# Kernel optimization log

Measured on AMD Instinct MI355X. Metric: run time of the kernel, lower is better.

Reference implementation:

```python
import jax, jax.numpy as jnp
import numpy as np

# heavy-atom counts minus 1 (the residue_len) for the 20 standard amino acids
# GLY ALA SER CYS THR VAL PRO LEU ILE ASN ASP MET GLN GLU LYS HIS PHE ARG TYR TRP
NATOMS = np.array([4,5,6,6,7,7,7,8,8,8,8,8,9,9,9,10,11,11,12,14], dtype=np.int64)
NTYPES = 20
MAXA = int(NATOMS.max())  # 14
B, R, VDIM, NLIN = 128, 512, 256, 3


def setup_inputs() -> dict:
    rng = np.random.default_rng(0)
    type_ids = rng.integers(0, NTYPES, size=R)                     # metadata.seq as type ids
    natoms = NATOMS[type_ids]                                      # per-residue atom count
    residue_indices = np.concatenate([[0], np.cumsum(natoms)[:-1]])  # start atom of each residue
    n_atoms = int(natoms.sum())

    key = jax.random.key(0)
    k1, k2, k3 = jax.random.split(key, 3)
    x = jax.random.normal(k1, (B, n_atoms, 3), dtype=jnp.float32)

    # per-type first-layer weight, zero-padded beyond each type's natom so the
    # padded gathered atoms contribute exactly zero (identical math to slicing)
    pad_mask = (np.arange(MAXA)[None, :] < NATOMS[:, None]).astype(np.float32)  # (T, A)
    W0 = jax.random.normal(k2, (NTYPES, VDIM, MAXA), dtype=jnp.float32)
    W0 = W0 * (1.0 / np.sqrt(MAXA)) * jnp.asarray(pad_mask)[:, None, :]
    Wh = jax.random.normal(k3, (NTYPES, NLIN - 1, VDIM, VDIM), dtype=jnp.float32) * (1.0 / np.sqrt(VDIM))

    return {
        "x": x,
        "W0": W0,
        "Wh": Wh,
        "type_ids": jnp.asarray(type_ids, dtype=jnp.int64),
        "residue_indices": jnp.asarray(residue_indices, dtype=jnp.int64),
    }


def reference(x, W0, Wh, type_ids, residue_indices):
    """x:(B, atoms, 3) -> pos_ca:(B, R, 3), x_v:(B, R, VDIM, 3)"""
    n_atoms = x.shape[1]
    # gather each residue's atom window, padded to MAXA (clip keeps indices in
    # range; padded entries are killed by the zero-padded W0 columns)
    atom_idx = jnp.clip(residue_indices[:, None] + jnp.arange(MAXA)[None, :], 0, n_atoms - 1)  # (R, A)
    gathered = x[:, atom_idx]                               # (B, R, A, 3)
    root = x[:, residue_indices + 1]                        # (B, R, 3)  -- CA atom (x[:,1] of each slice)
    delta = gathered - root[:, :, None, :]                  # subtract root

    h = jnp.einsum('rva,brac->brvc', W0[type_ids], delta)   # per-type VecLinear(natom -> vdim)
    for l in range(NLIN - 1):                               # per-type VecLinear(vdim -> vdim)
        h = jnp.einsum('rvu,bruc->brvc', Wh[type_ids, l], h)

    pos_ca = root                                            # x[:, residue_indices + 1]
    return pos_ca, h
```

## Files before the change

kernel.cpp:

```cpp
#include <hip/hip_runtime.h>

namespace {
constexpr int NB = 128;
constexpr int NR = 512;
constexpr int ND = 256;
constexpr int NA = 14;

using short8 = __attribute__((ext_vector_type(8))) short;
using f32x4  = __attribute__((ext_vector_type(4))) float;

constexpr size_t WH_US  = (size_t)40 * 16 * 8 * 64 * 8;
constexpr size_t W0_OFF = WH_US;
constexpr size_t W0_US  = (size_t)20 * 16 * 64 * 8;
constexpr size_t RMAP_BYTE_OFF = (WH_US + W0_US) * 2;
constexpr size_t WS_NEEDED = RMAP_BYTE_OFF + NR * sizeof(int);

__device__ __forceinline__ unsigned short f2bf(float f) {
    unsigned int u = __float_as_uint(f);
    u = (u + 0x7FFFu + ((u >> 16) & 1u)) >> 16;
    return (unsigned short)u;
}
}

__global__ void conv_wh(const float* __restrict__ Wh, unsigned short* __restrict__ ws) {
    int g = blockIdx.x * 256 + threadIdx.x;
    if (g >= 40 * 16 * 8 * 64) return;
    const int lane = g & 63, kt = (g >> 6) & 7, mt = (g >> 9) & 15, tl = g >> 13;
    const int v = mt * 16 + (lane & 15);
    const int u0 = kt * 32 + (lane >> 4) * 8;
    const float* src = Wh + ((size_t)tl * ND + v) * ND + u0;
    unsigned short o[8];
#pragma unroll
    for (int j = 0; j < 8; ++j) o[j] = f2bf(src[j]);
    uint4 pk;
    pk.x = o[0] | ((unsigned)o[1] << 16); pk.y = o[2] | ((unsigned)o[3] << 16);
    pk.z = o[4] | ((unsigned)o[5] << 16); pk.w = o[6] | ((unsigned)o[7] << 16);
    *reinterpret_cast<uint4*>(ws + (size_t)g * 8) = pk;
}

__global__ void conv_w0(const float* __restrict__ W0, unsigned short* __restrict__ ws) {
    int g = blockIdx.x * 256 + threadIdx.x;
    if (g >= 20 * 16 * 64) return;
    const int lane = g & 63, mt = (g >> 6) & 15, t = g >> 10;
    const int v = mt * 16 + (lane & 15);
    const int a0 = (lane >> 4) * 8;
    unsigned short o[8];
#pragma unroll
    for (int j = 0; j < 8; ++j) {
        const int a = a0 + j;
        o[j] = (a < NA) ? f2bf(W0[((size_t)t * ND + v) * NA + a]) : (unsigned short)0;
    }
    uint4 pk;
    pk.x = o[0] | ((unsigned)o[1] << 16); pk.y = o[2] | ((unsigned)o[3] << 16);
    pk.z = o[4] | ((unsigned)o[5] << 16); pk.w = o[6] | ((unsigned)o[7] << 16);
    *reinterpret_cast<uint4*>(ws + W0_OFF + (size_t)g * 8) = pk;
}

__global__ void build_rmap(const int* __restrict__ type_ids, int* __restrict__ rmap) {
    __shared__ int tl[NR];
    const int tid = threadIdx.x;
    tl[tid] = type_ids[tid];
    __syncthreads();
    const int myt = tl[tid];
    int pos = 0;
    for (int j = 0; j < NR; ++j) {
        const int tj = tl[j];
        pos += (tj < myt) || (tj == myt && j < tid);
    }
    rmap[pos] = tid;
}

__global__ __launch_bounds__(512, 6) void residues_mfma(
    const float* __restrict__ x, const unsigned short* __restrict__ wsw,
    const int* __restrict__ rmap, const int* __restrict__ type_ids,
    const int* __restrict__ res_idx, float* __restrict__ out, int n_atoms)
{
    const int tid = threadIdx.x, lane = tid & 63, w = tid >> 6;
    const int xcd = blockIdx.x & 7, j = blockIdx.x >> 3;
    const int r = rmap[xcd * 64 + (j >> 3)];
    const int b0 = (j & 7) * 16;
    const int ri = res_idx[r], t = type_ids[r];

    __shared__ __align__(16) unsigned short HT[48 * 264];
    unsigned short* dltT = HT;

    const unsigned short* w0b = wsw + W0_OFF + (size_t)t * (16 * 64 * 8);
    short8 a0[2];
#pragma unroll
    for (int mi = 0; mi < 2; ++mi)
        a0[mi] = *reinterpret_cast<const short8*>(w0b + (((w * 2 + mi) * 64) + lane) * 8);

    {
        const int bl = tid >> 5, k = tid & 31;
        const float* xb = x + (size_t)(b0 + bl) * n_atoms * 3;
        if (k < 16) {
            int atom = ri + k; if (atom > n_atoms - 1) atom = n_atoms - 1;
            const float* src  = xb + (size_t)atom * 3;
            const float* root = xb + (size_t)(ri + 1) * 3;
#pragma unroll
            for (int c = 0; c < 3; ++c)
                dltT[(bl * 3 + c) * 40 + k] = f2bf(src[c] - root[c]);
            if (k == 1) {
#pragma unroll
                for (int c = 0; c < 3; ++c)
                    out[((size_t)(b0 + bl) * NR + r) * 3 + c] = root[c];
            }
        } else {
#pragma unroll
            for (int c = 0; c < 3; ++c)
                dltT[(bl * 3 + c) * 40 + k] = 0;
        }
    }
    __syncthreads();

    f32x4 acc[2][3];
#pragma unroll
    for (int mi = 0; mi < 2; ++mi)
#pragma unroll
        for (int ni = 0; ni < 3; ++ni) acc[mi][ni] = f32x4{0.f, 0.f, 0.f, 0.f};

    {
        short8 bf[3];
#pragma unroll
        for (int ni = 0; ni < 3; ++ni)
            bf[ni] = *reinterpret_cast<const short8*>(&dltT[(ni * 16 + (lane & 15)) * 40 + (lane >> 4) * 8]);
#pragma unroll
        for (int mi = 0; mi < 2; ++mi)
#pragma unroll
            for (int ni = 0; ni < 3; ++ni)
                acc[mi][ni] = __builtin_amdgcn_mfma_f32_16x16x32_bf16(a0[mi], bf[ni], acc[mi][ni], 0, 0, 0);
    }
    __syncthreads();

#pragma unroll 1
    for (int l = 0; l < 2; ++l) {
#pragma unroll
        for (int mi = 0; mi < 2; ++mi)
#pragma unroll
            for (int ni = 0; ni < 3; ++ni) {
                const int v0 = w * 32 + mi * 16 + (lane >> 4) * 4;
                const int n  = ni * 16 + (lane & 15);
                const unsigned lo = (unsigned)f2bf(acc[mi][ni][0]) | ((unsigned)f2bf(acc[mi][ni][1]) << 16);
                const unsigned hi = (unsigned)f2bf(acc[mi][ni][2]) | ((unsigned)f2bf(acc[mi][ni][3]) << 16);
                *reinterpret_cast<uint2*>(&HT[n * 264 + v0]) = make_uint2(lo, hi);
            }
        __syncthreads();

#pragma unroll
        for (int mi = 0; mi < 2; ++mi)
#pragma unroll
            for (int ni = 0; ni < 3; ++ni) acc[mi][ni] = f32x4{0.f, 0.f, 0.f, 0.f};

        const unsigned short* wl = wsw + (size_t)(t * 2 + l) * (16 * 8 * 64 * 8);
#pragma unroll 1
        for (int kt = 0; kt < 8; ++kt) {
            short8 a[2], bf[3];
#pragma unroll
            for (int mi = 0; mi < 2; ++mi)
                a[mi] = *reinterpret_cast<const short8*>(wl + ((((w * 2 + mi) * 8 + kt) * 64) + lane) * 8);
#pragma unroll
            for (int ni = 0; ni < 3; ++ni)
                bf[ni] = *reinterpret_cast<const short8*>(&HT[(ni * 16 + (lane & 15)) * 264 + kt * 32 + (lane >> 4) * 8]);
#pragma unroll
            for (int mi = 0; mi < 2; ++mi)
#pragma unroll
                for (int ni = 0; ni < 3; ++ni)
                    acc[mi][ni] = __builtin_amdgcn_mfma_f32_16x16x32_bf16(a[mi], bf[ni], acc[mi][ni], 0, 0, 0);
        }
        if (l == 0) __syncthreads();
    }

    float* fst  = reinterpret_cast<float*>(HT);
    float* outh = out + (size_t)NB * NR * 3;
#pragma unroll 1
    for (int p = 0; p < 2; ++p) {
        __syncthreads();
        if ((w >> 2) == p) {
            const int wq = w & 3;
#pragma unroll
            for (int mi = 0; mi < 2; ++mi)
#pragma unroll
                for (int ni = 0; ni < 3; ++ni) {
                    const int n = ni * 16 + (lane & 15);
#pragma unroll
                    for (int jj = 0; jj < 4; ++jj) {
                        const int vl = wq * 32 + mi * 16 + (lane >> 4) * 4 + jj;
                        fst[n * 132 + vl] = acc[mi][ni][jj];
                    }
                }
        }
        __syncthreads();
#pragma unroll
        for (int i = 0; i < 3; ++i) {
            const int idx = tid + i * 512;
            const int bl = idx / 96, g = idx % 96;
            f32x4 v4;
#pragma unroll
            for (int e = 0; e < 4; ++e) {
                const int f = 4 * g + e, c = f % 3, vp = f / 3;
                v4[e] = fst[(bl * 3 + c) * 132 + vp];
            }
            __builtin_nontemporal_store(v4,
                reinterpret_cast<f32x4*>(&outh[(((size_t)(b0 + bl) * NR + r) * (ND * 3)) + p * 384 + 4 * g]));
        }
    }
}

__global__ __launch_bounds__(256, 3) void residues_fused_fb(
    const float* __restrict__ x, const float* __restrict__ W0,
    const float* __restrict__ Wh, const int* __restrict__ type_ids,
    const int* __restrict__ res_idx, float* __restrict__ out, int n_atoms)
{
    const int tid = threadIdx.x;
    const int r = blockIdx.x >> 4;
    const int b0 = (blockIdx.x & 15) * 8;
    const int ri = res_idx[r], t = type_ids[r];
    __shared__ float dlt[NA][24];
    __shared__ float hA[ND][24];
    __shared__ float hB[ND][24];
    for (int idx = tid; idx < 8 * NA * 3; idx += 256) {
        const int bb = idx / (NA * 3), rem = idx % (NA * 3);
        const int a = rem / 3, c = rem % 3, b = b0 + bb;
        int ca = ri + a; if (ca > n_atoms - 1) ca = n_atoms - 1;
        const float root = x[((size_t)b * n_atoms + (ri + 1)) * 3 + c];
        dlt[a][bb * 3 + c] = x[((size_t)b * n_atoms + ca) * 3 + c] - root;
        if (a == 0) out[((size_t)b * NR + r) * 3 + c] = root;
    }
    __syncthreads();
    {
        const float* w0row = W0 + ((size_t)t * ND + tid) * NA;
        float acc[24];
#pragma unroll
        for (int n = 0; n < 24; ++n) acc[n] = 0.f;
#pragma unroll
        for (int a = 0; a < NA; ++a) {
            const float wv = w0row[a];
#pragma unroll
            for (int n = 0; n < 24; ++n) acc[n] += wv * dlt[a][n];
        }
#pragma unroll
        for (int n = 0; n < 24; ++n) hA[tid][n] = acc[n];
    }
    __syncthreads();
    const float* whbase = Wh + (size_t)t * 2 * ND * ND;
#pragma unroll
    for (int l = 0; l < 2; ++l) {
        const float* wrow = whbase + ((size_t)l * ND + tid) * ND;
        const float (*hin)[24] = (l == 0) ? hA : hB;
        float (*hout)[24]      = (l == 0) ? hB : hA;
        float acc[24];
#pragma unroll
        for (int n = 0; n < 24; ++n) acc[n] = 0.f;
        for (int u = 0; u < ND; ++u) {
            const float wv = wrow[u];
#pragma unroll
            for (int n = 0; n < 24; ++n) acc[n] += wv * hin[u][n];
        }
#pragma unroll
        for (int n = 0; n < 24; ++n) hout[tid][n] = acc[n];
        __syncthreads();
    }
    float* outh = out + (size_t)NB * NR * 3;
#pragma unroll
    for (int bb = 0; bb < 8; ++bb) {
        const size_t base = ((size_t)((b0 + bb) * NR + r)) * (ND * 3);
#pragma unroll
        for (int it = 0; it < 3; ++it) {
            const int g = it * 256 + tid;
            outh[base + g] = hA[g / 3][bb * 3 + g % 3];
        }
    }
}

extern "C" void kernel_launch(void* const* d_in, const int* in_sizes, int n_in,
                              void* d_out, int out_size, void* d_ws, size_t ws_size,
                              hipStream_t stream) {
    const float* x        = (const float*)d_in[0];
    const float* W0       = (const float*)d_in[1];
    const float* Wh       = (const float*)d_in[2];
    const int*   type_ids = (const int*)d_in[3];
    const int*   res_idx  = (const int*)d_in[4];
    float* out = (float*)d_out;
    const int n_atoms = in_sizes[0] / (NB * 3);

    if (ws_size >= WS_NEEDED) {
        unsigned short* wsw = (unsigned short*)d_ws;
        int* rmap = (int*)((char*)d_ws + RMAP_BYTE_OFF);
        conv_wh<<<(40 * 16 * 8 * 64 + 255) / 256, 256, 0, stream>>>(Wh, wsw);
        conv_w0<<<(20 * 16 * 64 + 255) / 256, 256, 0, stream>>>(W0, wsw);
        build_rmap<<<1, NR, 0, stream>>>(type_ids, rmap);
        residues_mfma<<<NR * 8, 512, 0, stream>>>(x, wsw, rmap, type_ids, res_idx, out, n_atoms);
    } else {
        residues_fused_fb<<<NR * 16, 256, 0, stream>>>(x, W0, Wh, type_ids, res_idx, out, n_atoms);
    }
}
```

Baseline: 98.18 us.

## Merge prep kernels into one launch and single-pass swizzled output epilogue

The three preprocessing kernels (Wh bf16 conversion, W0 conversion, residue sort map) become one launch whose blocks branch by block index, removing two kernel launches. The MFMA kernel's epilogue now stages the full 48x256 fp32 tile in LDS in one pass, using vectorised f32x4 writes with an XOR swizzle to reduce bank conflicts. This replaces the old two-pass scheme that wrote scalars and needed extra barriers. In exchange the LDS footprint per block roughly doubles, which can lower the number of resident blocks per CU.

Result: slower. 108.1 us (+10.1%).

```diff
diff --git a/kernel.cpp b/kernel.cpp
--- a/kernel.cpp
+++ b/kernel.cpp
@@ -20,54 +20,58 @@
     u = (u + 0x7FFFu + ((u >> 16) & 1u)) >> 16;
     return (unsigned short)u;
 }
-}
-
-__global__ void conv_wh(const float* __restrict__ Wh, unsigned short* __restrict__ ws) {
-    int g = blockIdx.x * 256 + threadIdx.x;
-    if (g >= 40 * 16 * 8 * 64) return;
-    const int lane = g & 63, kt = (g >> 6) & 7, mt = (g >> 9) & 15, tl = g >> 13;
-    const int v = mt * 16 + (lane & 15);
-    const int u0 = kt * 32 + (lane >> 4) * 8;
-    const float* src = Wh + ((size_t)tl * ND + v) * ND + u0;
-    unsigned short o[8];
-#pragma unroll
-    for (int j = 0; j < 8; ++j) o[j] = f2bf(src[j]);
-    uint4 pk;
-    pk.x = o[0] | ((unsigned)o[1] << 16); pk.y = o[2] | ((unsigned)o[3] << 16);
-    pk.z = o[4] | ((unsigned)o[5] << 16); pk.w = o[6] | ((unsigned)o[7] << 16);
-    *reinterpret_cast<uint4*>(ws + (size_t)g * 8) = pk;
-}
-
-__global__ void conv_w0(const float* __restrict__ W0, unsigned short* __restrict__ ws) {
-    int g = blockIdx.x * 256 + threadIdx.x;
-    if (g >= 20 * 16 * 64) return;
-    const int lane = g & 63, mt = (g >> 6) & 15, t = g >> 10;
-    const int v = mt * 16 + (lane & 15);
-    const int a0 = (lane >> 4) * 8;
-    unsigned short o[8];
-#pragma unroll
-    for (int j = 0; j < 8; ++j) {
-        const int a = a0 + j;
-        o[j] = (a < NA) ? f2bf(W0[((size_t)t * ND + v) * NA + a]) : (unsigned short)0;
-    }
-    uint4 pk;
-    pk.x = o[0] | ((unsigned)o[1] << 16); pk.y = o[2] | ((unsigned)o[3] << 16);
-    pk.z = o[4] | ((unsigned)o[5] << 16); pk.w = o[6] | ((unsigned)o[7] << 16);
-    *reinterpret_cast<uint4*>(ws + W0_OFF + (size_t)g * 8) = pk;
-}
-
-__global__ void build_rmap(const int* __restrict__ type_ids, int* __restrict__ rmap) {
+__device__ __forceinline__ int vswz(int v) { return v ^ (((v >> 5) & 3) << 3); }
+}
+
+__global__ __launch_bounds__(256) void prep_all(
+    const float* __restrict__ Wh, const float* __restrict__ W0,
+    const int* __restrict__ type_ids,
+    unsigned short* __restrict__ ws, int* __restrict__ rmap)
+{
     __shared__ int tl[NR];
-    const int tid = threadIdx.x;
-    tl[tid] = type_ids[tid];
-    __syncthreads();
-    const int myt = tl[tid];
-    int pos = 0;
-    for (int j = 0; j < NR; ++j) {
-        const int tj = tl[j];
-        pos += (tj < myt) || (tj == myt && j < tid);
-    }
-    rmap[pos] = tid;
+    const int bid = blockIdx.x, tid = threadIdx.x;
+    if (bid < 1280) {
+        const int g = bid * 256 + tid;
+        const int lane = g & 63, kt = (g >> 6) & 7, mt = (g >> 9) & 15, tw = g >> 13;
+        const int v = mt * 16 + (lane & 15);
+        const int u0 = kt * 32 + (lane >> 4) * 8;
+        const float* src = Wh + ((size_t)tw * ND + v) * ND + u0;
+        unsigned short o[8];
+#pragma unroll
+        for (int j = 0; j < 8; ++j) o[j] = f2bf(src[j]);
+        uint4 pk;
+        pk.x = o[0] | ((unsigned)o[1] << 16); pk.y = o[2] | ((unsigned)o[3] << 16);
+        pk.z = o[4] | ((unsigned)o[5] << 16); pk.w = o[6] | ((unsigned)o[7] << 16);
+        *reinterpret_cast<uint4*>(ws + (size_t)g * 8) = pk;
+    } else if (bid < 1360) {
+        const int g = (bid - 1280) * 256 + tid;
+        const int lane = g & 63, mt = (g >> 6) & 15, t = g >> 10;
+        const int v = mt * 16 + (lane & 15);
+        const int a0 = (lane >> 4) * 8;
+        unsigned short o[8];
+#pragma unroll
+        for (int j = 0; j < 8; ++j) {
+            const int a = a0 + j;
+            o[j] = (a < NA) ? f2bf(W0[((size_t)t * ND + v) * NA + a]) : (unsigned short)0;
+        }
+        uint4 pk;
+        pk.x = o[0] | ((unsigned)o[1] << 16); pk.y = o[2] | ((unsigned)o[3] << 16);
+        pk.z = o[4] | ((unsigned)o[5] << 16); pk.w = o[6] | ((unsigned)o[7] << 16);
+        *reinterpret_cast<uint4*>(ws + W0_OFF + (size_t)g * 8) = pk;
+    } else {
+        tl[tid] = type_ids[tid];
+        tl[tid + 256] = type_ids[tid + 256];
+        __syncthreads();
+        for (int i = tid; i < NR; i += 256) {
+            const int myt = tl[i];
+            int pos = 0;
+            for (int j = 0; j < NR; ++j) {
+                const int tj = tl[j];
+                pos += (tj < myt) || (tj == myt && j < i);
+            }
+            rmap[pos] = i;
+        }
+    }
 }
 
 __global__ __launch_bounds__(512, 6) void residues_mfma(
@@ -81,8 +85,9 @@
     const int b0 = (j & 7) * 16;
     const int ri = res_idx[r], t = type_ids[r];
 
-    __shared__ __align__(16) unsigned short HT[48 * 264];
-    unsigned short* dltT = HT;
+    __shared__ __align__(16) float fst[48 * 260];
+    unsigned short* dltT = reinterpret_cast<unsigned short*>(fst);
+    unsigned short* HT   = reinterpret_cast<unsigned short*>(fst);
 
     const unsigned short* w0b = wsw + W0_OFF + (size_t)t * (16 * 64 * 8);
     short8 a0[2];
@@ -167,42 +172,33 @@
                 for (int ni = 0; ni < 3; ++ni)
                     acc[mi][ni] = __builtin_amdgcn_mfma_f32_16x16x32_bf16(a[mi], bf[ni], acc[mi][ni], 0, 0, 0);
         }
-        if (l == 0) __syncthreads();
-    }
-
-    float* fst  = reinterpret_cast<float*>(HT);
+        __syncthreads();
+    }
+
+#pragma unroll
+    for (int mi = 0; mi < 2; ++mi)
+#pragma unroll
+        for (int ni = 0; ni < 3; ++ni) {
+            const int n  = ni * 16 + (lane & 15);
+            const int vb = w * 32 + mi * 16 + (lane >> 4) * 4;
+            *reinterpret_cast<f32x4*>(&fst[n * 260 + vswz(vb)]) = acc[mi][ni];
+        }
+    __syncthreads();
+
     float* outh = out + (size_t)NB * NR * 3;
-#pragma unroll 1
-    for (int p = 0; p < 2; ++p) {
-        __syncthreads();
-        if ((w >> 2) == p) {
-            const int wq = w & 3;
-#pragma unroll
-            for (int mi = 0; mi < 2; ++mi)
-#pragma unroll
-                for (int ni = 0; ni < 3; ++ni) {
-                    const int n = ni * 16 + (lane & 15);
-#pragma unroll
-                    for (int jj = 0; jj < 4; ++jj) {
-                        const int vl = wq * 32 + mi * 16 + (lane >> 4) * 4 + jj;
-                        fst[n * 132 + vl] = acc[mi][ni][jj];
-                    }
-                }
-        }
-        __syncthreads();
-#pragma unroll
-        for (int i = 0; i < 3; ++i) {
-            const int idx = tid + i * 512;
-            const int bl = idx / 96, g = idx % 96;
-            f32x4 v4;
-#pragma unroll
-            for (int e = 0; e < 4; ++e) {
-                const int f = 4 * g + e, c = f % 3, vp = f / 3;
-                v4[e] = fst[(bl * 3 + c) * 132 + vp];
-            }
-            __builtin_nontemporal_store(v4,
-                reinterpret_cast<f32x4*>(&outh[(((size_t)(b0 + bl) * NR + r) * (ND * 3)) + p * 384 + 4 * g]));
-        }
+#pragma unroll
+    for (int i = 0; i < 6; ++i) {
+        const int idx = tid + i * 512;
+        const int bl = idx / 192;
+        const int fo = (idx % 192) * 4;
+        f32x4 v4;
+#pragma unroll
+        for (int e = 0; e < 4; ++e) {
+            const int f = fo + e, c = f % 3, vp = f / 3;
+            v4[e] = fst[(bl * 3 + c) * 260 + vswz(vp)];
+        }
+        __builtin_nontemporal_store(v4,
+            reinterpret_cast<f32x4*>(&outh[(((size_t)(b0 + bl) * NR + r) * (ND * 3)) + fo]));
     }
 }
 
@@ -286,9 +282,7 @@
     if (ws_size >= WS_NEEDED) {
         unsigned short* wsw = (unsigned short*)d_ws;
         int* rmap = (int*)((char*)d_ws + RMAP_BYTE_OFF);
-        conv_wh<<<(40 * 16 * 8 * 64 + 255) / 256, 256, 0, stream>>>(Wh, wsw);
-        conv_w0<<<(20 * 16 * 64 + 255) / 256, 256, 0, stream>>>(W0, wsw);
-        build_rmap<<<1, NR, 0, stream>>>(type_ids, rmap);
+        prep_all<<<1361, 256, 0, stream>>>(Wh, W0, type_ids, wsw, rmap);
         residues_mfma<<<NR * 8, 512, 0, stream>>>(x, wsw, rmap, type_ids, res_idx, out, n_atoms);
     } else {
         residues_fused_fb<<<NR * 16, 256, 0, stream>>>(x, W0, Wh, type_ids, res_idx, out, n_atoms);
```
